# Kernel tuning notes

Measured on AMD Instinct MI355X. Metric: run time of the kernel, lower is better.

## Reference

```python
import jax, jax.numpy as jnp
import numpy as np

E = 200000          # number of edges (nodes of the line graph)
NNZ = 1600000       # nonzeros of the edge-to-edge sparse adjacency
EF = 16             # edge_feat_dim
M = 128             # message_dim


def setup_inputs() -> dict:
    key = jax.random.key(0)
    ks = jax.random.split(key, 12)
    inp = {
        "edge_feat": jax.random.normal(ks[0], (E, EF), jnp.float32),
        "message_old": jax.random.normal(ks[1], (E, M), jnp.float32),
        "adj_rows": jax.random.randint(ks[2], (NNZ,), 0, E, jnp.int32),
        "adj_cols": jax.random.randint(ks[3], (NNZ,), 0, E, jnp.int32),
        "adj_vals": jax.random.uniform(ks[4], (NNZ,), jnp.float32),
        # message_edge_lin: Linear(EF+M -> M)
        "W1": jax.random.normal(ks[5], (M, EF + M), jnp.float32) / np.sqrt(EF + M),
        "b1": jnp.zeros((M,), jnp.float32),
        # message_pass_lin: Linear(M -> M)
        "W2": jax.random.normal(ks[6], (M, M), jnp.float32) / np.sqrt(M),
        "b2": jnp.zeros((M,), jnp.float32),
        # GRUCell(M, M)
        "W_ih": jax.random.normal(ks[7], (3 * M, M), jnp.float32) / np.sqrt(M),
        "W_hh": jax.random.normal(ks[8], (3 * M, M), jnp.float32) / np.sqrt(M),
        "b_ih": jax.random.normal(ks[9], (3 * M,), jnp.float32) * 0.01,
        "b_hh": jax.random.normal(ks[10], (3 * M,), jnp.float32) * 0.01,
    }
    return inp


def reference(edge_feat, message_old, adj_rows, adj_cols, adj_vals,
              W1, b1, W2, b2, W_ih, W_hh, b_ih, b_hh):
    # message_edge_lin(cat(message_old, edge_feat)) + ReLU
    x = jnp.concatenate([message_old, edge_feat], axis=1)      # [E, M+EF]
    msg = jax.nn.relu(x @ W1.T + b1)                           # [E, M]
    # torch.sparse.mm(nb_adj, msg): out[r] += val * msg[c]
    gathered = msg[adj_cols] * adj_vals[:, None]               # [NNZ, M]
    msg = jax.ops.segment_sum(gathered, adj_rows, num_segments=E)
    # message_pass_lin + ReLU
    msg = jax.nn.relu(msg @ W2.T + b2)                         # [E, M]
    # GRUCell(input=msg, hidden=message_old), torch semantics
    gi = msg @ W_ih.T + b_ih                                   # [E, 3M]
    gh = message_old @ W_hh.T + b_hh                           # [E, 3M]
    i_r, i_z, i_n = jnp.split(gi, 3, axis=1)
    h_r, h_z, h_n = jnp.split(gh, 3, axis=1)
    r = jax.nn.sigmoid(i_r + h_r)
    z = jax.nn.sigmoid(i_z + h_z)
    n = jnp.tanh(i_n + r * h_n)
    return (1.0 - z) * n + z * message_old
```

## Files before the change

kernel.cpp:

```cpp
#include <hip/hip_runtime.h>
#include <hip/hip_bf16.h>


typedef __attribute__((ext_vector_type(4))) float f32x4;
typedef __attribute__((ext_vector_type(8))) short s16x8;

#define MDIM 128
#define EFDIM 16
#define K1PAD 160
#define SCAN_BLK 1024

__device__ __forceinline__ ushort f2bf(float f) {
  union { float f; unsigned u; } v; v.f = f;
  unsigned u = v.u;
  unsigned r = (u + 0x7fffu + ((u >> 16) & 1u)) >> 16;
  return (ushort)r;
}
__device__ __forceinline__ float bf2f(ushort h) {
  union { unsigned u; float f; } v; v.u = ((unsigned)h) << 16; return v.f;
}
__device__ __forceinline__ s16x8 cvt8(f32x4 a, f32x4 b) {
  s16x8 o;
  o[0] = (short)f2bf(a[0]); o[1] = (short)f2bf(a[1]);
  o[2] = (short)f2bf(a[2]); o[3] = (short)f2bf(a[3]);
  o[4] = (short)f2bf(b[0]); o[5] = (short)f2bf(b[1]);
  o[6] = (short)f2bf(b[2]); o[7] = (short)f2bf(b[3]);
  return o;
}
__device__ __forceinline__ f32x4 mfma16(s16x8 a, s16x8 b, f32x4 c) {
  return __builtin_amdgcn_mfma_f32_16x16x32_bf16(a, b, c, 0, 0, 0);
}
__device__ __forceinline__ float sigmoidf_(float x) { return 1.f / (1.f + __expf(-x)); }
__device__ __forceinline__ float tanhf_(float x) {
  float xc = fminf(fmaxf(x, -15.f), 15.f);
  float t = __expf(2.f * xc);
  return (t - 1.f) / (t + 1.f);
}

__global__ __launch_bounds__(256) void prep_kernel(
    const float* __restrict__ W1, const float* __restrict__ W2,
    const float* __restrict__ Wih, const float* __restrict__ Whh,
    ushort* __restrict__ W1b, ushort* __restrict__ W2b,
    ushort* __restrict__ Wihb, ushort* __restrict__ Whhb) {
  int idx = blockIdx.x * 256 + threadIdx.x;
  if (idx < 128 * K1PAD) {
    int n = idx / K1PAD, k = idx % K1PAD;
    W1b[idx] = (k < 144) ? f2bf(W1[n * 144 + k]) : (ushort)0;
    return;
  }
  int i2 = idx - 128 * K1PAD;
  if (i2 < 128 * 128) { W2b[i2] = f2bf(W2[i2]); return; }
  int i3 = i2 - 128 * 128;
  if (i3 < 384 * 128) { Wihb[i3] = f2bf(Wih[i3]); return; }
  int i4 = i3 - 384 * 128;
  if (i4 < 384 * 128) { Whhb[i4] = f2bf(Whh[i4]); return; }
}

__global__ __launch_bounds__(256) void linear1_kernel(
    const float* __restrict__ mo, const float* __restrict__ ef,
    const ushort* __restrict__ W1b, const float* __restrict__ b1,
    ushort* __restrict__ msg1b) {
  __shared__ ushort w1l[128 * 192];
  const int tid = threadIdx.x;
  const int wave = tid >> 6, lane = tid & 63;
  const int r = lane & 15, kg = lane >> 4;
  const int row0 = blockIdx.x * 64 + wave * 16;
  const int arow = row0 + r;

#pragma unroll
  for (int l = 0; l < 10; ++l) {
    const int gid = l * 256 + tid;
    const int row = gid / 20, g = gid - row * 20;
    uint4 v = *(const uint4*)(W1b + row * K1PAD + g * 8);
    *(uint4*)&w1l[row * 192 + ((g ^ (row & 7)) * 8)] = v;
  }
  __syncthreads();

  f32x4 acc[8] = {};
#pragma unroll
  for (int step = 0; step < 5; ++step) {
    const int k0 = step * 32 + kg * 8;
    s16x8 a;
    if (k0 < 128) {
      f32x4 f1 = *(const f32x4*)(mo + (size_t)arow * MDIM + k0);
      f32x4 f2 = *(const f32x4*)(mo + (size_t)arow * MDIM + k0 + 4);
      a = cvt8(f1, f2);
    } else if (k0 < 144) {
      f32x4 f1 = *(const f32x4*)(ef + (size_t)arow * EFDIM + (k0 - 128));
      f32x4 f2 = *(const f32x4*)(ef + (size_t)arow * EFDIM + (k0 - 128) + 4);
      a = cvt8(f1, f2);
    } else {
      a = (s16x8){0, 0, 0, 0, 0, 0, 0, 0};
    }
#pragma unroll
    for (int f = 0; f < 8; ++f) {
      const int col = f * 16 + r;
      s16x8 b = *(const s16x8*)&w1l[col * 192 + (((step * 4 + kg) ^ (col & 7)) * 8)];
      acc[f] = mfma16(a, b, acc[f]);
    }
  }
#pragma unroll
  for (int f = 0; f < 8; ++f) {
    const int col = f * 16 + r;
    const float bias = b1[col];
#pragma unroll
    for (int j = 0; j < 4; ++j) {
      const int orow = row0 + kg * 4 + j;
      float v = acc[f][j] + bias;
      v = v > 0.f ? v : 0.f;
      msg1b[(size_t)orow * MDIM + col] = f2bf(v);
    }
  }
}

__global__ __launch_bounds__(256) void hist_kernel(const int* __restrict__ rows,
                                                   int* __restrict__ cnt, int nnz) {
  int i = blockIdx.x * 256 + threadIdx.x;
  if (i < nnz) atomicAdd(&cnt[rows[i]], 1);
}

__global__ __launch_bounds__(256) void scan1_kernel(const int* __restrict__ cnt,
                                                    int* __restrict__ excl,
                                                    int* __restrict__ bsums, int n) {
  __shared__ int wsum[4];
  const int t = threadIdx.x;
  const int base = blockIdx.x * SCAN_BLK + t * 4;
  int v[4];
#pragma unroll
  for (int j = 0; j < 4; ++j) v[j] = (base + j < n) ? cnt[base + j] : 0;
  const int s = v[0] + v[1] + v[2] + v[3];
  const int lane = t & 63, wave = t >> 6;
  int inc = s;
#pragma unroll
  for (int d = 1; d < 64; d <<= 1) {
    int o = __shfl_up(inc, d, 64);
    if (lane >= d) inc += o;
  }
  if (lane == 63) wsum[wave] = inc;
  __syncthreads();
  int woff = 0;
#pragma unroll
  for (int wv = 0; wv < 4; ++wv) if (wv < wave) woff += wsum[wv];
  int run = woff + inc - s;
#pragma unroll
  for (int j = 0; j < 4; ++j) {
    if (base + j < n) excl[base + j] = run;
    run += v[j];
  }
  if (t == 0) bsums[blockIdx.x] = wsum[0] + wsum[1] + wsum[2] + wsum[3];
}

__global__ __launch_bounds__(256) void scan2_kernel(int* __restrict__ bsums, int nb) {
  __shared__ int ws[4];
  const int t = threadIdx.x;
  const int v = (t < nb) ? bsums[t] : 0;
  const int lane = t & 63, wave = t >> 6;
  int inc = v;
#pragma unroll
  for (int d = 1; d < 64; d <<= 1) {
    int o = __shfl_up(inc, d, 64);
    if (lane >= d) inc += o;
  }
  if (lane == 63) ws[wave] = inc;
  __syncthreads();
  int woff = 0;
#pragma unroll
  for (int wv = 0; wv < 4; ++wv) if (wv < wave) woff += ws[wv];
  if (t < nb) bsums[t] = woff + inc - v;
}

__global__ __launch_bounds__(256) void scan3_kernel(int* __restrict__ row_ptr,
                                                    int* __restrict__ row_fill,
                                                    const int* __restrict__ bsums, int n) {
  int i = blockIdx.x * 256 + threadIdx.x;
  if (i >= n) return;
  int v = row_ptr[i] + bsums[i / SCAN_BLK];
  row_ptr[i] = v;
  row_fill[i] = v;
}

__global__ __launch_bounds__(256) void scatter_kernel(
    const int* __restrict__ rows, const int* __restrict__ cols,
    const float* __restrict__ vals, int* __restrict__ row_fill,
    int2* __restrict__ csr, int nnz) {
  int i = blockIdx.x * 256 + threadIdx.x;
  if (i >= nnz) return;
  int r = rows[i];
  int idx = atomicAdd(&row_fill[r], 1);
  int2 cv;
  cv.x = cols[i];
  cv.y = __float_as_int(vals[i]);
  csr[idx] = cv;
}

__global__ __launch_bounds__(256) void gather_kernel(
    const int* __restrict__ row_ptr, const int2* __restrict__ csr,
    const ushort* __restrict__ msg1b, ushort* __restrict__ msg2b,
    int E, int nnz) {
  const int w = (blockIdx.x * 256 + threadIdx.x) >> 6;
  if (w >= E) return;
  const int lane = threadIdx.x & 63;
  const int sub = lane >> 4, c = lane & 15;
  const int start = row_ptr[w];
  const int end = (w == E - 1) ? nnz : row_ptr[w + 1];

  float acc[8] = {};
  int j = start + sub;
  if (j < end) {
    int2 cv = csr[j];
    while (true) {
      const int jn = j + 4;
      const bool more = jn < end;
      int2 cvn = cv;
      if (more) cvn = csr[jn];
      const float val = __int_as_float(cv.y);
      const s16x8 m = *(const s16x8*)(msg1b + (size_t)cv.x * MDIM + c * 8);
#pragma unroll
      for (int t = 0; t < 8; ++t) acc[t] += bf2f((ushort)m[t]) * val;
      if (!more) break;
      cv = cvn;
      j = jn;
    }
  }
#pragma unroll
  for (int t = 0; t < 8; ++t) {
    acc[t] += __shfl_xor(acc[t], 16, 64);
    acc[t] += __shfl_xor(acc[t], 32, 64);
  }
  if (sub == 0) {
    s16x8 o;
#pragma unroll
    for (int t = 0; t < 8; ++t) o[t] = (short)f2bf(acc[t]);
    *(s16x8*)(msg2b + (size_t)w * MDIM + c * 8) = o;
  }
}

__global__ __launch_bounds__(256) void msg3_kernel(
    const ushort* __restrict__ msg2b, const ushort* __restrict__ W2b,
    const float* __restrict__ b2, ushort* __restrict__ msg3b) {
  __shared__ ushort w2l[128 * 128];
  const int tid = threadIdx.x;
  const int wave = tid >> 6, lane = tid & 63;
  const int r = lane & 15, kg = lane >> 4;
  const int row0 = blockIdx.x * 64 + wave * 16;

#pragma unroll
  for (int l = 0; l < 8; ++l) {
    const int gid = l * 256 + tid;
    const int row = gid >> 4, g = gid & 15;
    uint4 v = *(const uint4*)(W2b + row * MDIM + g * 8);
    *(uint4*)&w2l[row * 128 + ((g * 8) ^ ((row & 7) << 3))] = v;
  }

  s16x8 a1[4];
#pragma unroll
  for (int step = 0; step < 4; ++step)
    a1[step] = *(const s16x8*)(msg2b + (size_t)(row0 + r) * MDIM + step * 32 + kg * 8);
  __syncthreads();

  f32x4 acc[8] = {};
#pragma unroll
  for (int step = 0; step < 4; ++step) {
    const int k0 = step * 32 + kg * 8;
#pragma unroll
    for (int f = 0; f < 8; ++f) {
      const int col = f * 16 + r;
      s16x8 b = *(const s16x8*)&w2l[col * 128 + (k0 ^ ((col & 7) << 3))];
      acc[f] = mfma16(a1[step], b, acc[f]);
    }
  }
#pragma unroll
  for (int f = 0; f < 8; ++f) {
    const int col = f * 16 + r;
    const float bias = b2[col];
#pragma unroll
    for (int j = 0; j < 4; ++j) {
      const int orow = row0 + kg * 4 + j;
      float v = acc[f][j] + bias;
      v = v > 0.f ? v : 0.f;
      msg3b[(size_t)orow * MDIM + col] = f2bf(v);
    }
  }
}

__global__ __launch_bounds__(512, 4) void gate_kernel(
    const ushort* __restrict__ msg3b, const float* __restrict__ mo,
    const ushort* __restrict__ Wihb, const ushort* __restrict__ Whhb,
    const float* __restrict__ bih, const float* __restrict__ bhh,
    float* __restrict__ out, int E) {
  __shared__ ushort wl[6 * 4096];
  const int tid = threadIdx.x;

  const int nwg = gridDim.x;
  const int orig = blockIdx.x;
  const int q = nwg >> 3, rm = nwg & 7;
  const int xcd = orig & 7, idx = orig >> 3;
  const int wgid = (xcd < rm ? xcd * (q + 1) : rm * (q + 1) + (xcd - rm) * q) + idx;
  const int cg = wgid & 3;
  const int row0 = (wgid >> 2) * 128;

  const int wave = tid >> 6, lane = tid & 63;
  const int r = lane & 15, kg = lane >> 4;

  const int lr = tid >> 4, g = tid & 15;
#pragma unroll
  for (int l = 0; l < 6; ++l) {
    const ushort* src = (l & 1) ? Whhb : Wihb;
    const int gate = l >> 1;
    uint4 v = *(const uint4*)(src + (size_t)(gate * 128 + cg * 32 + lr) * MDIM + g * 8);
    *(uint4*)&wl[l * 4096 + lr * 128 + ((g * 8) ^ ((lr & 7) << 3))] = v;
  }

  const int arow0 = row0 + wave * 16 + r;
  const int arow = arow0 < E ? arow0 : E - 1;
  s16x8 ai[4], ah[4];
#pragma unroll
  for (int step = 0; step < 4; ++step) {
    const int k0 = step * 32 + kg * 8;
    ai[step] = *(const s16x8*)(msg3b + (size_t)arow * MDIM + k0);
    f32x4 f1 = *(const f32x4*)(mo + (size_t)arow * MDIM + k0);
    f32x4 f2 = *(const f32x4*)(mo + (size_t)arow * MDIM + k0 + 4);
    ah[step] = cvt8(f1, f2);
  }
  __syncthreads();

  float outv[8];
#pragma unroll
  for (int p = 0; p < 2; ++p) {
    const int slr = p * 16 + r;
    f32x4 a_ir = {}, a_hr = {}, a_iz = {}, a_hz = {}, a_in = {}, a_hn = {};
#pragma unroll
    for (int step = 0; step < 4; ++step) {
      const int k0 = step * 32 + kg * 8;
      const int sw = slr * 128 + (k0 ^ ((slr & 7) << 3));
      s16x8 b_ir = *(const s16x8*)&wl[0 * 4096 + sw];
      s16x8 b_hr = *(const s16x8*)&wl[1 * 4096 + sw];
      a_ir = mfma16(ai[step], b_ir, a_ir);
      a_hr = mfma16(ah[step], b_hr, a_hr);
      s16x8 b_iz = *(const s16x8*)&wl[2 * 4096 + sw];
      s16x8 b_hz = *(const s16x8*)&wl[3 * 4096 + sw];
      a_iz = mfma16(ai[step], b_iz, a_iz);
      a_hz = mfma16(ah[step], b_hz, a_hz);
      s16x8 b_in = *(const s16x8*)&wl[4 * 4096 + sw];
      s16x8 b_hn = *(const s16x8*)&wl[5 * 4096 + sw];
      a_in = mfma16(ai[step], b_in, a_in);
      a_hn = mfma16(ah[step], b_hn, a_hn);
    }
    const int c128 = cg * 32 + p * 16 + r;
    const float bi_r = bih[c128], bh_r = bhh[c128];
    const float bi_z = bih[128 + c128], bh_z = bhh[128 + c128];
    const float bi_n = bih[256 + c128], bh_n = bhh[256 + c128];
#pragma unroll
    for (int j = 0; j < 4; ++j) {
      const int orow0 = row0 + wave * 16 + kg * 4 + j;
      const int orow = orow0 < E ? orow0 : E - 1;
      const float rr_ = sigmoidf_((a_ir[j] + bi_r) + (a_hr[j] + bh_r));
      const float zz = sigmoidf_((a_iz[j] + bi_z) + (a_hz[j] + bh_z));
      const float nn = tanhf_((a_in[j] + bi_n) + rr_ * (a_hn[j] + bh_n));
      const float m = mo[(size_t)orow * MDIM + c128];
      outv[p * 4 + j] = (1.f - zz) * nn + zz * m;
    }
  }

#pragma unroll
  for (int p = 0; p < 2; ++p) {
    const int c128 = cg * 32 + p * 16 + r;
#pragma unroll
    for (int j = 0; j < 4; ++j) {
      const int orow = row0 + wave * 16 + kg * 4 + j;
      if (orow < E)
        __builtin_nontemporal_store(outv[p * 4 + j], out + (size_t)orow * MDIM + c128);
    }
  }
}

extern "C" void kernel_launch(void* const* d_in, const int* in_sizes, int n_in,
                              void* d_out, int out_size, void* d_ws, size_t ws_size,
                              hipStream_t stream) {
  const float* ef   = (const float*)d_in[0];
  const float* mo   = (const float*)d_in[1];
  const int*   arow = (const int*)d_in[2];
  const int*   acol = (const int*)d_in[3];
  const float* aval = (const float*)d_in[4];
  const float* W1   = (const float*)d_in[5];
  const float* b1   = (const float*)d_in[6];
  const float* W2   = (const float*)d_in[7];
  const float* b2   = (const float*)d_in[8];
  const float* Wih  = (const float*)d_in[9];
  const float* Whh  = (const float*)d_in[10];
  const float* bih  = (const float*)d_in[11];
  const float* bhh  = (const float*)d_in[12];
  float* out = (float*)d_out;

  const int E   = in_sizes[0] / EFDIM;
  const int nnz = in_sizes[2];

  char* w = (char*)d_ws;
  size_t off = 0;
  ushort* msg1b   = (ushort*)(w + off); off += (size_t)E * MDIM * 2;
  ushort* msg2b   = (ushort*)(w + off); off += (size_t)E * MDIM * 2;
  ushort* msg3b   = (ushort*)(w + off); off += (size_t)E * MDIM * 2;
  int*    row_cnt = (int*)(w + off);    off += (size_t)E * 4;
  int*    row_ptr = (int*)(w + off);    off += (size_t)E * 4;
  int*    row_fill= (int*)(w + off);    off += (size_t)E * 4;
  int*    bsums   = (int*)(w + off);    off += 256 * 4;
  int2*   csr     = (int2*)(w + off);   off += (size_t)nnz * 8;
  ushort* W1b     = (ushort*)(w + off); off += 128 * K1PAD * 2;
  ushort* W2b     = (ushort*)(w + off); off += 128 * 128 * 2;
  ushort* Wihb    = (ushort*)(w + off); off += 384 * 128 * 2;
  ushort* Whhb    = (ushort*)(w + off); off += 384 * 128 * 2;
  if (off > ws_size) return;

  const int prep_elems = 128 * K1PAD + 128 * 128 + 2 * 384 * 128;
  prep_kernel<<<(prep_elems + 255) / 256, 256, 0, stream>>>(W1, W2, Wih, Whh,
                                                            W1b, W2b, Wihb, Whhb);
  linear1_kernel<<<E / 64, 256, 0, stream>>>(mo, ef, W1b, b1, msg1b);

  hipMemsetAsync(row_cnt, 0, (size_t)E * 4, stream);
  hist_kernel<<<(nnz + 255) / 256, 256, 0, stream>>>(arow, row_cnt, nnz);
  const int nscan = (E + SCAN_BLK - 1) / SCAN_BLK;
  scan1_kernel<<<nscan, 256, 0, stream>>>(row_cnt, row_ptr, bsums, E);
  scan2_kernel<<<1, 256, 0, stream>>>(bsums, nscan);
  scan3_kernel<<<(E + 255) / 256, 256, 0, stream>>>(row_ptr, row_fill, bsums, E);
  scatter_kernel<<<(nnz + 255) / 256, 256, 0, stream>>>(arow, acol, aval, row_fill, csr, nnz);

  {
    const long long total = (long long)E * 64;
    const int grid = (int)((total + 255) / 256);
    gather_kernel<<<grid, 256, 0, stream>>>(row_ptr, csr, msg1b, msg2b, E, nnz);
  }

  msg3_kernel<<<E / 64, 256, 0, stream>>>(msg2b, W2b, b2, msg3b);
  {
    const int nrt = (E + 127) / 128;
    gate_kernel<<<nrt * 4, 512, 0, stream>>>(msg3b, mo, Wihb, Whhb, bih, bhh, out, E);
  }
}
```

Measured before the change: 450.2 us.

## Fold scan3 into scatter/gather and make gate kernel persistent

Removes the scan3 pass by computing row offsets on the fly as the exclusive scan plus block sum in both scatter and gather. row_fill now starts at zero, with the memset widened to cover row_cnt and row_fill. The gate kernel becomes a persistent grid of 1024 blocks that loads its weight slice into LDS once and loops over row tiles, with biases hoisted and the mo loads issued early. This saves a launch and repeated weight staging, at the cost of extra index math and less parallelism per tile.

```diff
diff --git a/kernel.cpp b/kernel.cpp
--- a/kernel.cpp
+++ b/kernel.cpp
@@ -169,24 +169,16 @@
   if (t < nb) bsums[t] = woff + inc - v;
 }
 
-__global__ __launch_bounds__(256) void scan3_kernel(int* __restrict__ row_ptr,
-                                                    int* __restrict__ row_fill,
-                                                    const int* __restrict__ bsums, int n) {
-  int i = blockIdx.x * 256 + threadIdx.x;
-  if (i >= n) return;
-  int v = row_ptr[i] + bsums[i / SCAN_BLK];
-  row_ptr[i] = v;
-  row_fill[i] = v;
-}
-
 __global__ __launch_bounds__(256) void scatter_kernel(
     const int* __restrict__ rows, const int* __restrict__ cols,
-    const float* __restrict__ vals, int* __restrict__ row_fill,
+    const float* __restrict__ vals, const int* __restrict__ excl,
+    const int* __restrict__ bsums, int* __restrict__ row_fill,
     int2* __restrict__ csr, int nnz) {
   int i = blockIdx.x * 256 + threadIdx.x;
   if (i >= nnz) return;
   int r = rows[i];
-  int idx = atomicAdd(&row_fill[r], 1);
+  int base = excl[r] + bsums[r >> 10];
+  int idx = base + atomicAdd(&row_fill[r], 1);
   int2 cv;
   cv.x = cols[i];
   cv.y = __float_as_int(vals[i]);
@@ -194,15 +186,16 @@
 }
 
 __global__ __launch_bounds__(256) void gather_kernel(
-    const int* __restrict__ row_ptr, const int2* __restrict__ csr,
+    const int* __restrict__ excl, const int* __restrict__ bsums,
+    const int2* __restrict__ csr,
     const ushort* __restrict__ msg1b, ushort* __restrict__ msg2b,
     int E, int nnz) {
   const int w = (blockIdx.x * 256 + threadIdx.x) >> 6;
   if (w >= E) return;
   const int lane = threadIdx.x & 63;
   const int sub = lane >> 4, c = lane & 15;
-  const int start = row_ptr[w];
-  const int end = (w == E - 1) ? nnz : row_ptr[w + 1];
+  const int start = excl[w] + bsums[w >> 10];
+  const int end = (w + 1 < E) ? (excl[w + 1] + bsums[(w + 1) >> 10]) : nnz;
 
   float acc[8] = {};
   int j = start + sub;
@@ -287,17 +280,15 @@
     const ushort* __restrict__ msg3b, const float* __restrict__ mo,
     const ushort* __restrict__ Wihb, const ushort* __restrict__ Whhb,
     const float* __restrict__ bih, const float* __restrict__ bhh,
-    float* __restrict__ out, int E) {
+    float* __restrict__ out, int E, int ntiles) {
   __shared__ ushort wl[6 * 4096];
   const int tid = threadIdx.x;
-
-  const int nwg = gridDim.x;
-  const int orig = blockIdx.x;
-  const int q = nwg >> 3, rm = nwg & 7;
-  const int xcd = orig & 7, idx = orig >> 3;
-  const int wgid = (xcd < rm ? xcd * (q + 1) : rm * (q + 1) + (xcd - rm) * q) + idx;
-  const int cg = wgid & 3;
-  const int row0 = (wgid >> 2) * 128;
+  const int bid = blockIdx.x;
+  const int xcd = bid & 7;
+  const int slot = bid >> 3;
+  const int cg = slot & 3;
+  const int chunk = xcd + ((slot >> 2) << 3);
+  const int NCHUNK = (int)(gridDim.x >> 2);
 
   const int wave = tid >> 6, lane = tid & 63;
   const int r = lane & 15, kg = lane >> 4;
@@ -311,65 +302,74 @@
     *(uint4*)&wl[l * 4096 + lr * 128 + ((g * 8) ^ ((lr & 7) << 3))] = v;
   }
 
-  const int arow0 = row0 + wave * 16 + r;
-  const int arow = arow0 < E ? arow0 : E - 1;
-  s16x8 ai[4], ah[4];
-#pragma unroll
-  for (int step = 0; step < 4; ++step) {
-    const int k0 = step * 32 + kg * 8;
-    ai[step] = *(const s16x8*)(msg3b + (size_t)arow * MDIM + k0);
-    f32x4 f1 = *(const f32x4*)(mo + (size_t)arow * MDIM + k0);
-    f32x4 f2 = *(const f32x4*)(mo + (size_t)arow * MDIM + k0 + 4);
-    ah[step] = cvt8(f1, f2);
+  float bi_r[2], bh_r[2], bi_z[2], bh_z[2], bi_n[2], bh_n[2];
+#pragma unroll
+  for (int p = 0; p < 2; ++p) {
+    const int c128 = cg * 32 + p * 16 + r;
+    bi_r[p] = bih[c128];       bh_r[p] = bhh[c128];
+    bi_z[p] = bih[128 + c128]; bh_z[p] = bhh[128 + c128];
+    bi_n[p] = bih[256 + c128]; bh_n[p] = bhh[256 + c128];
   }
   __syncthreads();
 
-  float outv[8];
-#pragma unroll
-  for (int p = 0; p < 2; ++p) {
-    const int slr = p * 16 + r;
-    f32x4 a_ir = {}, a_hr = {}, a_iz = {}, a_hz = {}, a_in = {}, a_hn = {};
+  for (int t = chunk; t < ntiles; t += NCHUNK) {
+    const int row0 = t * 128;
+    const int arow0 = row0 + wave * 16 + r;
+    const int arow = arow0 < E ? arow0 : E - 1;
+
+    s16x8 ai[4], ah[4];
+    float mo_m[2][4];
 #pragma unroll
     for (int step = 0; step < 4; ++step) {
       const int k0 = step * 32 + kg * 8;
-      const int sw = slr * 128 + (k0 ^ ((slr & 7) << 3));
-      s16x8 b_ir = *(const s16x8*)&wl[0 * 4096 + sw];
-      s16x8 b_hr = *(const s16x8*)&wl[1 * 4096 + sw];
-      a_ir = mfma16(ai[step], b_ir, a_ir);
-      a_hr = mfma16(ah[step], b_hr, a_hr);
-      s16x8 b_iz = *(const s16x8*)&wl[2 * 4096 + sw];
-      s16x8 b_hz = *(const s16x8*)&wl[3 * 4096 + sw];
-      a_iz = mfma16(ai[step], b_iz, a_iz);
-      a_hz = mfma16(ah[step], b_hz, a_hz);
-      s16x8 b_in = *(const s16x8*)&wl[4 * 4096 + sw];
-      s16x8 b_hn = *(const s16x8*)&wl[5 * 4096 + sw];
-      a_in = mfma16(ai[step], b_in, a_in);
-      a_hn = mfma16(ah[step], b_hn, a_hn);
-    }
-    const int c128 = cg * 32 + p * 16 + r;
-    const float bi_r = bih[c128], bh_r = bhh[c128];
-    const float bi_z = bih[128 + c128], bh_z = bhh[128 + c128];
-    const float bi_n = bih[256 + c128], bh_n = bhh[256 + c128];
-#pragma unroll
-    for (int j = 0; j < 4; ++j) {
-      const int orow0 = row0 + wave * 16 + kg * 4 + j;
-      const int orow = orow0 < E ? orow0 : E - 1;
-      const float rr_ = sigmoidf_((a_ir[j] + bi_r) + (a_hr[j] + bh_r));
-      const float zz = sigmoidf_((a_iz[j] + bi_z) + (a_hz[j] + bh_z));
-      const float nn = tanhf_((a_in[j] + bi_n) + rr_ * (a_hn[j] + bh_n));
-      const float m = mo[(size_t)orow * MDIM + c128];
-      outv[p * 4 + j] = (1.f - zz) * nn + zz * m;
-    }
-  }
-
-#pragma unroll
-  for (int p = 0; p < 2; ++p) {
-    const int c128 = cg * 32 + p * 16 + r;
-#pragma unroll
-    for (int j = 0; j < 4; ++j) {
-      const int orow = row0 + wave * 16 + kg * 4 + j;
-      if (orow < E)
-        __builtin_nontemporal_store(outv[p * 4 + j], out + (size_t)orow * MDIM + c128);
+      ai[step] = *(const s16x8*)(msg3b + (size_t)arow * MDIM + k0);
+      f32x4 f1 = *(const f32x4*)(mo + (size_t)arow * MDIM + k0);
+      f32x4 f2 = *(const f32x4*)(mo + (size_t)arow * MDIM + k0 + 4);
+      ah[step] = cvt8(f1, f2);
+    }
+#pragma unroll
+    for (int p = 0; p < 2; ++p) {
+      const int c128 = cg * 32 + p * 16 + r;
+#pragma unroll
+      for (int j = 0; j < 4; ++j) {
+        const int orow0 = row0 + wave * 16 + kg * 4 + j;
+        const int orow = orow0 < E ? orow0 : E - 1;
+        mo_m[p][j] = mo[(size_t)orow * MDIM + c128];
+      }
+    }
+
+#pragma unroll
+    for (int p = 0; p < 2; ++p) {
+      const int slr = p * 16 + r;
+      f32x4 a_ir = {}, a_hr = {}, a_iz = {}, a_hz = {}, a_in = {}, a_hn = {};
+#pragma unroll
+      for (int step = 0; step < 4; ++step) {
+        const int k0 = step * 32 + kg * 8;
+        const int sw = slr * 128 + (k0 ^ ((slr & 7) << 3));
+        s16x8 b_ir = *(const s16x8*)&wl[0 * 4096 + sw];
+        s16x8 b_hr = *(const s16x8*)&wl[1 * 4096 + sw];
+        a_ir = mfma16(ai[step], b_ir, a_ir);
+        a_hr = mfma16(ah[step], b_hr, a_hr);
+        s16x8 b_iz = *(const s16x8*)&wl[2 * 4096 + sw];
+        s16x8 b_hz = *(const s16x8*)&wl[3 * 4096 + sw];
+        a_iz = mfma16(ai[step], b_iz, a_iz);
+        a_hz = mfma16(ah[step], b_hz, a_hz);
+        s16x8 b_in = *(const s16x8*)&wl[4 * 4096 + sw];
+        s16x8 b_hn = *(const s16x8*)&wl[5 * 4096 + sw];
+        a_in = mfma16(ai[step], b_in, a_in);
+        a_hn = mfma16(ah[step], b_hn, a_hn);
+      }
+      const int c128 = cg * 32 + p * 16 + r;
+#pragma unroll
+      for (int j = 0; j < 4; ++j) {
+        const int orow = row0 + wave * 16 + kg * 4 + j;
+        const float rr_ = sigmoidf_((a_ir[j] + bi_r[p]) + (a_hr[j] + bh_r[p]));
+        const float zz = sigmoidf_((a_iz[j] + bi_z[p]) + (a_hz[j] + bh_z[p]));
+        const float nn = tanhf_((a_in[j] + bi_n[p]) + rr_ * (a_hn[j] + bh_n[p]));
+        const float o = (1.f - zz) * nn + zz * mo_m[p][j];
+        if (orow < E)
+          __builtin_nontemporal_store(o, out + (size_t)orow * MDIM + c128);
+      }
     }
   }
 }
@@ -401,8 +401,8 @@
   ushort* msg2b   = (ushort*)(w + off); off += (size_t)E * MDIM * 2;
   ushort* msg3b   = (ushort*)(w + off); off += (size_t)E * MDIM * 2;
   int*    row_cnt = (int*)(w + off);    off += (size_t)E * 4;
-  int*    row_ptr = (int*)(w + off);    off += (size_t)E * 4;
   int*    row_fill= (int*)(w + off);    off += (size_t)E * 4;
+  int*    excl    = (int*)(w + off);    off += (size_t)E * 4;
   int*    bsums   = (int*)(w + off);    off += 256 * 4;
   int2*   csr     = (int2*)(w + off);   off += (size_t)nnz * 8;
   ushort* W1b     = (ushort*)(w + off); off += 128 * K1PAD * 2;
@@ -416,23 +416,23 @@
                                                             W1b, W2b, Wihb, Whhb);
   linear1_kernel<<<E / 64, 256, 0, stream>>>(mo, ef, W1b, b1, msg1b);
 
-  hipMemsetAsync(row_cnt, 0, (size_t)E * 4, stream);
+  hipMemsetAsync(row_cnt, 0, (size_t)E * 8, stream);
   hist_kernel<<<(nnz + 255) / 256, 256, 0, stream>>>(arow, row_cnt, nnz);
   const int nscan = (E + SCAN_BLK - 1) / SCAN_BLK;
-  scan1_kernel<<<nscan, 256, 0, stream>>>(row_cnt, row_ptr, bsums, E);
+  scan1_kernel<<<nscan, 256, 0, stream>>>(row_cnt, excl, bsums, E);
   scan2_kernel<<<1, 256, 0, stream>>>(bsums, nscan);
-  scan3_kernel<<<(E + 255) / 256, 256, 0, stream>>>(row_ptr, row_fill, bsums, E);
-  scatter_kernel<<<(nnz + 255) / 256, 256, 0, stream>>>(arow, acol, aval, row_fill, csr, nnz);
+  scatter_kernel<<<(nnz + 255) / 256, 256, 0, stream>>>(arow, acol, aval, excl, bsums,
+                                                        row_fill, csr, nnz);
 
   {
     const long long total = (long long)E * 64;
     const int grid = (int)((total + 255) / 256);
-    gather_kernel<<<grid, 256, 0, stream>>>(row_ptr, csr, msg1b, msg2b, E, nnz);
+    gather_kernel<<<grid, 256, 0, stream>>>(excl, bsums, csr, msg1b, msg2b, E, nnz);
   }
 
   msg3_kernel<<<E / 64, 256, 0, stream>>>(msg2b, W2b, b2, msg3b);
   {
-    const int nrt = (E + 127) / 128;
-    gate_kernel<<<nrt * 4, 512, 0, stream>>>(msg3b, mo, Wihb, Whhb, bih, bhh, out, E);
-  }
-}
+    const int ntiles = (E + 127) / 128;
+    gate_kernel<<<1024, 512, 0, stream>>>(msg3b, mo, Wihb, Whhb, bih, bhh, out, E, ntiles);
+  }
+}
```

After: 855.3 us. +90.0%, slower.
